# Optimization experiments

Measured on AMD Instinct MI355X. Metric: run time of the kernel, lower is better.

The kernel has to match this reference:

```python
import jax, jax.numpy as jnp
import numpy as np

B, S, D = 1, 2048, 2048
H = 16
Q_LORA = 1536
KV_LORA = 512
NOPE = 128
ROPE = 64
VD = 128
QHD = NOPE + ROPE  # 192
THETA = 50000.0
EPS = 1e-6


def rmsnorm(x, w, eps=EPS):
    xf = x.astype(jnp.float32)
    var = jnp.mean(xf * xf, axis=-1, keepdims=True)
    return (w * (xf * jax.lax.rsqrt(var + eps)).astype(x.dtype))


def rotate_half(x):
    x1, x2 = jnp.split(x, 2, axis=-1)
    return jnp.concatenate([-x2, x1], axis=-1)


def deinterleave(x):
    # view(..., d//2, 2).transpose(-1,-2).reshape(..., d): [x0,x2,...,x1,x3,...]
    b, h, s, d = x.shape
    return x.reshape(b, h, s, d // 2, 2).swapaxes(-1, -2).reshape(b, h, s, d)


def setup_inputs() -> dict:
    key = jax.random.key(0)
    ks = jax.random.split(key, 8)
    sc = 0.02
    return {
        "hidden_states": jax.random.normal(ks[0], (B, S, D), jnp.float32),
        "position_ids": jnp.broadcast_to(jnp.arange(S, dtype=jnp.int32), (B, S)),
        "q_a_w": jax.random.normal(ks[1], (Q_LORA, D), jnp.float32) * sc,
        "q_a_ln_w": jnp.ones((Q_LORA,), jnp.float32),
        "q_b_w": jax.random.normal(ks[2], (H * QHD, Q_LORA), jnp.float32) * sc,
        "kv_a_w": jax.random.normal(ks[3], (KV_LORA + ROPE, D), jnp.float32) * sc,
        "kv_a_ln_w": jnp.ones((KV_LORA,), jnp.float32),
        "kv_b_w": jax.random.normal(ks[4], (H * (NOPE + VD), KV_LORA), jnp.float32) * sc,
        "o_w": jax.random.normal(ks[5], (D, H * VD), jnp.float32) * sc,
    }


def reference(hidden_states, position_ids, q_a_w, q_a_ln_w, q_b_w, kv_a_w, kv_a_ln_w, kv_b_w, o_w):
    bsz, q_len, _ = hidden_states.shape
    # low-rank Q: q_b(rmsnorm(q_a(x)))
    q = rmsnorm(hidden_states @ q_a_w.T, q_a_ln_w) @ q_b_w.T
    q = q.reshape(bsz, q_len, H, QHD).transpose(0, 2, 1, 3)  # [b,h,s,192]
    q_nope, q_pe = q[..., :NOPE], q[..., NOPE:]
    # compressed KV + shared rope key
    ckv = hidden_states @ kv_a_w.T  # [b,s,512+64]
    compressed_kv, k_pe = ckv[..., :KV_LORA], ckv[..., KV_LORA:]
    k_pe = k_pe.reshape(bsz, q_len, 1, ROPE).transpose(0, 2, 1, 3)  # [b,1,s,64]
    kv = rmsnorm(compressed_kv, kv_a_ln_w) @ kv_b_w.T
    kv = kv.reshape(bsz, q_len, H, NOPE + VD).transpose(0, 2, 1, 3)
    k_nope, value_states = kv[..., :NOPE], kv[..., NOPE:]
    # rotary cache
    inv_freq = 1.0 / (THETA ** (jnp.arange(0, ROPE, 2, dtype=jnp.float32) / ROPE))
    t = jnp.arange(q_len, dtype=jnp.float32)
    freqs = jnp.outer(t, inv_freq)
    emb = jnp.concatenate([freqs, freqs], axis=-1)  # [s,64]
    cos = jnp.cos(emb)[position_ids][:, None]  # [b,1,s,64]
    sin = jnp.sin(emb)[position_ids][:, None]
    q_pe = deinterleave(q_pe)
    k_pe = deinterleave(k_pe)
    q_pe = q_pe * cos + rotate_half(q_pe) * sin
    k_pe = k_pe * cos + rotate_half(k_pe) * sin
    query_states = jnp.concatenate([q_nope, q_pe], axis=-1)  # [b,h,s,192]
    key_states = jnp.concatenate([k_nope, jnp.broadcast_to(k_pe, (bsz, H, q_len, ROPE))], axis=-1)
    scale = QHD ** (-0.5)
    scores = jnp.einsum('bhqd,bhkd->bhqk', query_states, key_states) * scale
    causal = jnp.tril(jnp.ones((q_len, q_len), bool))
    scores = jnp.where(causal, scores, jnp.finfo(scores.dtype).min)
    attn = jax.nn.softmax(scores, axis=-1)
    out = jnp.einsum('bhqk,bhkd->bhqd', attn, value_states)  # [b,h,s,128]
    out = out.transpose(0, 2, 1, 3).reshape(bsz, q_len, H * VD)
    return out @ o_w.T
```

## Files before the change

### kernel.cpp

```cpp
#include <hip/hip_runtime.h>
#include <hip/hip_bf16.h>
#include <cmath>

#define S_LEN 2048
#define D_MODEL 2048
#define N_HEADS 16
#define Q_LORA 1536
#define KV_LORA 512
#define NOPE 128
#define ROPE_D 64
#define VD 128
#define QHD 192
#define AC_W 2112

typedef __attribute__((ext_vector_type(8))) short bf16x8;
typedef __attribute__((ext_vector_type(4))) float f32x4;
typedef __attribute__((ext_vector_type(4))) unsigned short u16x4;

static __device__ __forceinline__ unsigned short f2u(float x) {
  union { float f; unsigned u; } v; v.f = x;
  unsigned r = v.u + 0x7fffu + ((v.u >> 16) & 1u);
  return (unsigned short)(r >> 16);
}
static __device__ __forceinline__ unsigned short f2u_fast(float x) {
  union { float f; unsigned u; } v; v.f = x;
  return (unsigned short)((v.u + 0x8000u) >> 16);
}
static __device__ __forceinline__ float u2f(unsigned short x) {
  union { unsigned u; float f; } v; v.u = ((unsigned)x) << 16;
  return v.f;
}

#define AS1 __attribute__((address_space(1)))
#define AS3 __attribute__((address_space(3)))
static __device__ __forceinline__ void gload_lds16(const unsigned short* g, unsigned short* l) {
  __builtin_amdgcn_global_load_lds((const AS1 unsigned int*)g, (AS3 unsigned int*)l, 16, 0, 0);
}

__global__ __launch_bounds__(256) void conv_all(const float* __restrict__ hidden,
                                                const float* __restrict__ qaw,
                                                const float* __restrict__ kvaw,
                                                const float* __restrict__ qbw,
                                                const float* __restrict__ kvbw,
                                                unsigned short* __restrict__ Hb,
                                                unsigned short* __restrict__ wbuf,
                                                unsigned short* __restrict__ qbwb,
                                                unsigned short* __restrict__ kvbwb,
                                                float qscale) {
  const int nH   = (S_LEN * D_MODEL) / 4;
  const int nQA  = (Q_LORA * D_MODEL) / 4;
  const int nKVA = ((KV_LORA + ROPE_D) * D_MODEL) / 4;
  const int nQB  = (N_HEADS * QHD * Q_LORA) / 4;
  const int nKVB = (N_HEADS * 256 * KV_LORA) / 4;
  const int e1 = nH, e2 = e1 + nQA + nKVA, e3 = e2 + nQB, e4 = e3 + nKVB;
  for (int i = blockIdx.x * 256 + threadIdx.x; i < e4; i += gridDim.x * 256) {
    float4 v;
    unsigned short* dst;
    int o;
    float sc = 1.f;
    if (i < e1) {
      o = i; v = ((const float4*)hidden)[o]; dst = Hb;
    } else if (i < e2) {
      o = i - e1;
      v = (o < nQA) ? ((const float4*)qaw)[o] : ((const float4*)kvaw)[o - nQA];
      dst = wbuf;
    } else if (i < e3) {
      o = i - e2; v = ((const float4*)qbw)[o]; dst = qbwb; sc = qscale;
    } else {
      o = i - e3; v = ((const float4*)kvbw)[o]; dst = kvbwb;
    }
    u16x4 u;
    u[0] = f2u(v.x * sc); u[1] = f2u(v.y * sc);
    u[2] = f2u(v.z * sc); u[3] = f2u(v.w * sc);
    ((u16x4*)dst)[o] = u;
  }
}

template <int MODE>
__global__ __launch_bounds__(256) void gemm_mfma(const unsigned short* __restrict__ A,
                                                 const unsigned short* __restrict__ W,
                                                 void* __restrict__ Cv,
                                                 int N, int K) {
  __shared__ unsigned short As[2][8192];
  __shared__ unsigned short Ws[2][4096];
  const int tid = threadIdx.x;
  const int wave = tid >> 6, lane = tid & 63;
  const int col16 = lane & 15, g = lane >> 4;
  const int arow = blockIdx.y * 128, wrow = blockIdx.x * 64;
  const int wm = (wave >> 1) * 64, wn = (wave & 1) * 32;

  const unsigned short* gA[4];
  const unsigned short* gW[2];
  int dA[4], dW[2];
#pragma unroll
  for (int i = 0; i < 4; ++i) {
    const int c = i * 256 + tid;
    const int r = c >> 3, sl = c & 7;
    gA[i] = A + (size_t)(arow + r) * K + (sl ^ (r & 7)) * 8;
    dA[i] = c * 8;
  }
#pragma unroll
  for (int i = 0; i < 2; ++i) {
    const int c = i * 256 + tid;
    const int r = c >> 3, sl = c & 7;
    gW[i] = W + (size_t)(wrow + r) * K + (sl ^ (r & 7)) * 8;
    dW[i] = c * 8;
  }

  f32x4 acc[4][2];
#pragma unroll
  for (int i = 0; i < 4; ++i)
#pragma unroll
    for (int j = 0; j < 2; ++j) acc[i][j] = (f32x4){0.f, 0.f, 0.f, 0.f};

#pragma unroll
  for (int i = 0; i < 4; ++i) gload_lds16(gA[i], &As[0][dA[i]]);
#pragma unroll
  for (int i = 0; i < 2; ++i) gload_lds16(gW[i], &Ws[0][dW[i]]);

  int cur = 0;
  for (int k0 = 0; k0 < K; k0 += 64) {
    __syncthreads();
    if (k0 + 64 < K) {
      const int b = cur ^ 1, kk = k0 + 64;
#pragma unroll
      for (int i = 0; i < 4; ++i) gload_lds16(gA[i] + kk, &As[b][dA[i]]);
#pragma unroll
      for (int i = 0; i < 2; ++i) gload_lds16(gW[i] + kk, &Ws[b][dW[i]]);
    }
#pragma unroll
    for (int kh = 0; kh < 2; ++kh) {
      bf16x8 af[4], bfr[2];
#pragma unroll
      for (int i = 0; i < 4; ++i) {
        const int row = wm + i * 16 + col16;
        af[i] = *(const bf16x8*)(&As[cur][row * 64 + (((kh * 4 + g) ^ (row & 7)) * 8)]);
      }
#pragma unroll
      for (int j = 0; j < 2; ++j) {
        const int row = wn + j * 16 + col16;
        bfr[j] = *(const bf16x8*)(&Ws[cur][row * 64 + (((kh * 4 + g) ^ (row & 7)) * 8)]);
      }
#pragma unroll
      for (int i = 0; i < 4; ++i)
#pragma unroll
        for (int j = 0; j < 2; ++j)
          acc[i][j] = __builtin_amdgcn_mfma_f32_16x16x32_bf16(af[i], bfr[j], acc[i][j], 0, 0, 0);
    }
    cur ^= 1;
  }

#pragma unroll
  for (int i = 0; i < 4; ++i)
#pragma unroll
    for (int j = 0; j < 2; ++j) {
      const int col = wrow + wn + j * 16 + col16;
      const int row0 = arow + wm + i * 16 + g * 4;
#pragma unroll
      for (int r = 0; r < 4; ++r) {
        if constexpr (MODE == 0)
          ((float*)Cv)[(size_t)(row0 + r) * N + col] = acc[i][j][r];
        else
          ((unsigned short*)Cv)[(size_t)(row0 + r) * N + col] = f2u(acc[i][j][r]);
      }
    }
}

__global__ __launch_bounds__(256) void gemm_qkv(const unsigned short* __restrict__ qan,
                                                const unsigned short* __restrict__ wq,
                                                unsigned short* __restrict__ qbuf,
                                                const unsigned short* __restrict__ ckvn,
                                                const unsigned short* __restrict__ wkv,
                                                unsigned short* __restrict__ Kb,
                                                unsigned short* __restrict__ Vt) {
  __shared__ unsigned short As[2][8192];
  __shared__ unsigned short Ws[2][4096];
  const int tid = threadIdx.x;
  const int wave = tid >> 6, lane = tid & 63;
  const int col16 = lane & 15, g = lane >> 4;
  const int bid = (int)blockIdx.x;
  const bool isQ = bid < 768;
  int bx, by;
  if (isQ) { bx = bid % 48; by = bid / 48; }
  else { const int r = bid - 768; bx = r & 63; by = r >> 6; }
  const int K = isQ ? Q_LORA : KV_LORA;
  const unsigned short* A = isQ ? qan : ckvn;
  const unsigned short* W = isQ ? wq : wkv;
  const int arow = by * 128, wrow = bx * 64;
  const int wm = (wave >> 1) * 64, wn = (wave & 1) * 32;

  const unsigned short* gA[4];
  const unsigned short* gW[2];
  int dA[4], dW[2];
#pragma unroll
  for (int i = 0; i < 4; ++i) {
    const int c = i * 256 + tid;
    const int r = c >> 3, sl = c & 7;
    gA[i] = A + (size_t)(arow + r) * K + (sl ^ (r & 7)) * 8;
    dA[i] = c * 8;
  }
#pragma unroll
  for (int i = 0; i < 2; ++i) {
    const int c = i * 256 + tid;
    const int r = c >> 3, sl = c & 7;
    gW[i] = W + (size_t)(wrow + r) * K + (sl ^ (r & 7)) * 8;
    dW[i] = c * 8;
  }

  f32x4 acc[4][2];
#pragma unroll
  for (int i = 0; i < 4; ++i)
#pragma unroll
    for (int j = 0; j < 2; ++j) acc[i][j] = (f32x4){0.f, 0.f, 0.f, 0.f};

#pragma unroll
  for (int i = 0; i < 4; ++i) gload_lds16(gA[i], &As[0][dA[i]]);
#pragma unroll
  for (int i = 0; i < 2; ++i) gload_lds16(gW[i], &Ws[0][dW[i]]);

  int cur = 0;
  for (int k0 = 0; k0 < K; k0 += 64) {
    __syncthreads();
    if (k0 + 64 < K) {
      const int b = cur ^ 1, kk = k0 + 64;
#pragma unroll
      for (int i = 0; i < 4; ++i) gload_lds16(gA[i] + kk, &As[b][dA[i]]);
#pragma unroll
      for (int i = 0; i < 2; ++i) gload_lds16(gW[i] + kk, &Ws[b][dW[i]]);
    }
#pragma unroll
    for (int kh = 0; kh < 2; ++kh) {
      bf16x8 af[4], bfr[2];
#pragma unroll
      for (int i = 0; i < 4; ++i) {
        const int row = wm + i * 16 + col16;
        af[i] = *(const bf16x8*)(&As[cur][row * 64 + (((kh * 4 + g) ^ (row & 7)) * 8)]);
      }
#pragma unroll
      for (int j = 0; j < 2; ++j) {
        const int row = wn + j * 16 + col16;
        bfr[j] = *(const bf16x8*)(&Ws[cur][row * 64 + (((kh * 4 + g) ^ (row & 7)) * 8)]);
      }
#pragma unroll
      for (int i = 0; i < 4; ++i)
#pragma unroll
        for (int j = 0; j < 2; ++j)
          acc[i][j] = __builtin_amdgcn_mfma_f32_16x16x32_bf16(af[i], bfr[j], acc[i][j], 0, 0, 0);
    }
    cur ^= 1;
  }

#pragma unroll
  for (int i = 0; i < 4; ++i)
#pragma unroll
    for (int j = 0; j < 2; ++j) {
      const int col = wrow + wn + j * 16 + col16;
      const int row0 = arow + wm + i * 16 + g * 4;
      if (isQ) {
#pragma unroll
        for (int r = 0; r < 4; ++r)
          qbuf[(size_t)(row0 + r) * (N_HEADS * QHD) + col] = f2u(acc[i][j][r]);
      } else {
        const int hh = col >> 8, d = col & 255;
        if (d < NOPE) {
#pragma unroll
          for (int r = 0; r < 4; ++r)
            Kb[((size_t)hh * S_LEN + row0 + r) * QHD + d] = f2u(acc[i][j][r]);
        } else {
          const int dv = d - NOPE;
          const int p0 = ((row0 & 15) >> 2) * 8 + ((row0 >> 4) & 1) * 4;
          u16x4 w4;
#pragma unroll
          for (int r = 0; r < 4; ++r) w4[r] = f2u(acc[i][j][r]);
          *(uint2*)(Vt + ((size_t)hh * VD + dv) * S_LEN + (row0 & ~31) + p0) =
              __builtin_bit_cast(uint2, w4);
        }
      }
    }
}

__global__ __launch_bounds__(256) void rmsnorm2_kernel(const unsigned short* __restrict__ ac,
                                                       const float* __restrict__ wq,
                                                       const float* __restrict__ wkv,
                                                       unsigned short* __restrict__ qan,
                                                       unsigned short* __restrict__ ckvn) {
  const int row = blockIdx.x;
  const bool kv = blockIdx.y != 0;
  const unsigned short* x = ac + (size_t)row * AC_W + (kv ? Q_LORA : 0);
  const float* w = kv ? wkv : wq;
  unsigned short* dst = kv ? (ckvn + (size_t)row * KV_LORA) : (qan + (size_t)row * Q_LORA);
  const int dim = kv ? KV_LORA : Q_LORA;
  float ss = 0.f;
  for (int i0 = threadIdx.x * 8; i0 < dim; i0 += 2048) {
    const bf16x8 v = *(const bf16x8*)(x + i0);
#pragma unroll
    for (int e = 0; e < 8; ++e) {
      const float f = u2f((unsigned short)v[e]);
      ss += f * f;
    }
  }
#pragma unroll
  for (int off = 32; off; off >>= 1) ss += __shfl_xor(ss, off);
  __shared__ float red[4];
  const int wv = threadIdx.x >> 6, ln = threadIdx.x & 63;
  if (ln == 0) red[wv] = ss;
  __syncthreads();
  const float tot = red[0] + red[1] + red[2] + red[3];
  const float scale = rsqrtf(tot / (float)dim + 1e-6f);
  for (int i0 = threadIdx.x * 8; i0 < dim; i0 += 2048) {
    const bf16x8 v = *(const bf16x8*)(x + i0);
    u16x4 o0, o1;
#pragma unroll
    for (int e = 0; e < 4; ++e) {
      o0[e] = f2u(w[i0 + e] * (u2f((unsigned short)v[e]) * scale));
      o1[e] = f2u(w[i0 + 4 + e] * (u2f((unsigned short)v[4 + e]) * scale));
    }
    *(uint2*)(dst + i0) = __builtin_bit_cast(uint2, o0);
    *(uint2*)(dst + i0 + 4) = __builtin_bit_cast(uint2, o1);
  }
}

__global__ __launch_bounds__(256) void rope_kernel(unsigned short* __restrict__ q,
                                                   const unsigned short* __restrict__ ac,
                                                   unsigned short* __restrict__ Kb,
                                                   const int* __restrict__ pos_ids) {
  const int s = blockIdx.x * 8 + (threadIdx.x >> 5);
  const int j = threadIdx.x & 31;
  const float t = (float)pos_ids[s];
  const float invf = powf(50000.0f, -(float)(2 * j) / 64.0f);
  const float ang = t * invf;
  const float c = cosf(ang), sn = sinf(ang);
#pragma unroll
  for (int h = 0; h < N_HEADS; ++h) {
    unsigned short* base = q + (size_t)s * (N_HEADS * QHD) + h * QHD + NOPE;
    const float x0 = u2f(base[2 * j]), x1 = u2f(base[2 * j + 1]);
    base[j] = f2u(x0 * c - x1 * sn);
    base[32 + j] = f2u(x1 * c + x0 * sn);
  }
  const unsigned short* kb = ac + (size_t)s * AC_W + 2048;
  const float kb0 = u2f(kb[2 * j]), kb1 = u2f(kb[2 * j + 1]);
  const unsigned short r0 = f2u(kb0 * c - kb1 * sn);
  const unsigned short r1 = f2u(kb1 * c + kb0 * sn);
#pragma unroll
  for (int h = 0; h < N_HEADS; ++h) {
    unsigned short* kd = Kb + ((size_t)h * S_LEN + s) * QHD + NOPE;
    kd[j] = r0;
    kd[32 + j] = r1;
  }
}

__global__ __launch_bounds__(256, 4) void flash_attn(const unsigned short* __restrict__ Q,
                                                     const unsigned short* __restrict__ Kb,
                                                     const unsigned short* __restrict__ Vt,
                                                     unsigned short* __restrict__ Pb,
                                                     float2* __restrict__ mlb) {
  __shared__ unsigned short Ks[2][32 * QHD];
  __shared__ unsigned short Vs[2][VD * 32];
  const int tid = threadIdx.x;
  const int wave = tid >> 6, lane = tid & 63;
  const int g = lane >> 4, col = lane & 15;
  const int lin = (int)blockIdx.x;
  const int h = ((lin & 7) << 1) | ((lin >> 3) & 1);
  const int s = (lin >> 4) & 1;
  const int z = lin >> 5;
  int t;
  if (z < 8) t = 31 - z;
  else if (z < 16) t = z - 8;
  else if (z < 24) t = 39 - z;
  else t = z - 16;
  const int qw = t * 64 + wave * 16;
  const int qr = qw + col;

  bf16x8 qf[6];
  {
    const unsigned short* qrow = Q + (size_t)qr * (N_HEADS * QHD) + h * QHD + g * 8;
#pragma unroll
    for (int i = 0; i < 6; ++i) qf[i] = *(const bf16x8*)(qrow + i * 32);
  }

  const unsigned short* KbH = Kb + (size_t)h * S_LEN * QHD;
  const unsigned short* VtH = Vt + (size_t)h * VD * S_LEN;

  int eK[3], eV[2];
#pragma unroll
  for (int i = 0; i < 3; ++i) {
    const int c = i * 256 + tid;
    const int r = c / 24, sl = c - r * 24;
    eK[i] = r * QHD + (((sl & 24) | ((sl & 7) ^ (r & 7)))) * 8;
  }
#pragma unroll
  for (int i = 0; i < 2; ++i) {
    const int L = i * 256 + tid;
    const int r = L >> 3, p = L & 7;
    const int px = p ^ (r & 7);
    const int d = 2 * r + (px >> 2), sl = px & 3;
    eV[i] = d * S_LEN + sl * 8;
  }

  f32x4 o[8];
#pragma unroll
  for (int i = 0; i < 8; ++i) o[i] = (f32x4){0.f, 0.f, 0.f, 0.f};
  float m = -1e30f, l = 0.f;

  const int nT = t + 1;

  {
    const unsigned short* kp = KbH + (size_t)s * 32 * QHD;
    const unsigned short* vp = VtH + s * 32;
#pragma unroll
    for (int i = 0; i < 3; ++i) gload_lds16(kp + eK[i], &Ks[0][(i * 256 + tid) * 8]);
#pragma unroll
    for (int i = 0; i < 2; ++i) gload_lds16(vp + eV[i], &Vs[0][(i * 256 + tid) * 8]);
  }

  int xK[6];
#pragma unroll
  for (int i = 0; i < 6; ++i) xK[i] = ((4 * i + g) ^ (col & 7)) * 8;
  const int rbK = col * QHD;
  const int vlane = (col >> 1) * 64 + ((((col & 1) << 2) + g) ^ (col >> 1)) * 8;

  for (int it = 0; it < nT; ++it) {
    __syncthreads();
    if (it + 1 < nT) {
      const int jn = 2 * (it + 1) + s;
      const unsigned short* kp = KbH + (size_t)jn * 32 * QHD;
      const unsigned short* vp = VtH + jn * 32;
      const int b = (it + 1) & 1;
#pragma unroll
      for (int i = 0; i < 3; ++i) gload_lds16(kp + eK[i], &Ks[b][(i * 256 + tid) * 8]);
#pragma unroll
      for (int i = 0; i < 2; ++i) gload_lds16(vp + eV[i], &Vs[b][(i * 256 + tid) * 8]);
    }
    const int k0 = 32 * (2 * it + s);
    if (k0 <= qw + 15) {
      const unsigned short* Ksc = Ks[it & 1];
      const unsigned short* Vsc = Vs[it & 1];

      f32x4 c0 = (f32x4){0.f, 0.f, 0.f, 0.f}, c1 = (f32x4){0.f, 0.f, 0.f, 0.f};
      __builtin_amdgcn_s_setprio(1);
#pragma unroll
      for (int dt = 0; dt < 6; ++dt) {
        const bf16x8 a0 = *(const bf16x8*)(Ksc + rbK + xK[dt]);
        const bf16x8 a1 = *(const bf16x8*)(Ksc + rbK + 16 * QHD + xK[dt]);
        c0 = __builtin_amdgcn_mfma_f32_16x16x32_bf16(a0, qf[dt], c0, 0, 0, 0);
        c1 = __builtin_amdgcn_mfma_f32_16x16x32_bf16(a1, qf[dt], c1, 0, 0, 0);
      }
      __builtin_amdgcn_s_setprio(0);

      if (k0 + 31 > qw) {
#pragma unroll
        for (int r = 0; r < 4; ++r) {
          const int kk = k0 + 4 * g + r;
          if (kk > qr) c0[r] = -1e30f;
          if (kk + 16 > qr) c1[r] = -1e30f;
        }
      }
      float bm = fmaxf(fmaxf(fmaxf(c0[0], c0[1]), fmaxf(c0[2], c0[3])),
                       fmaxf(fmaxf(c1[0], c1[1]), fmaxf(c1[2], c1[3])));
      bm = fmaxf(bm, __shfl_xor(bm, 16));
      bm = fmaxf(bm, __shfl_xor(bm, 32));
      const bool skip = __all(bm <= m + 8.f);
      const float mn = skip ? m : fmaxf(m, bm);
      float ps = 0.f;
      bf16x8 pb;
#pragma unroll
      for (int r = 0; r < 4; ++r) {
        const float p0 = exp2f(c0[r] - mn);
        const float p1 = exp2f(c1[r] - mn);
        ps += p0 + p1;
        pb[r] = (short)f2u_fast(p0);
        pb[4 + r] = (short)f2u_fast(p1);
      }
      ps += __shfl_xor(ps, 16);
      ps += __shfl_xor(ps, 32);
      if (skip) {
        l += ps;
      } else {
        const float corr = exp2f(m - mn);
        l = l * corr + ps;
        m = mn;
#pragma unroll
        for (int i = 0; i < 8; ++i) {
          o[i][0] *= corr; o[i][1] *= corr; o[i][2] *= corr; o[i][3] *= corr;
        }
      }
      __builtin_amdgcn_s_setprio(1);
#pragma unroll
      for (int db = 0; db < 8; ++db) {
        const bf16x8 va = *(const bf16x8*)(Vsc + db * 512 + vlane);
        o[db] = __builtin_amdgcn_mfma_f32_16x16x32_bf16(va, pb, o[db], 0, 0, 0);
      }
      __builtin_amdgcn_s_setprio(0);
    }
  }

  unsigned short* pr = Pb + (((size_t)qr * 2 + s) * N_HEADS + h) * VD;
#pragma unroll
  for (int db = 0; db < 8; ++db) {
    u16x4 w4;
#pragma unroll
    for (int r = 0; r < 4; ++r) w4[r] = f2u(o[db][r]);
    *(uint2*)(pr + db * 16 + 4 * g) = __builtin_bit_cast(uint2, w4);
  }
  if (g == 0) mlb[((size_t)qr * 2 + s) * N_HEADS + h] = make_float2(m, l);
}

__global__ __launch_bounds__(256) void combine2(const unsigned short* __restrict__ Pb,
                                                const float2* __restrict__ mlb,
                                                unsigned short* __restrict__ outb,
                                                const float* __restrict__ ow,
                                                unsigned short* __restrict__ owb) {
  const int nC = S_LEN * N_HEADS * VD / 8;
  const int nT = nC + (D_MODEL * N_HEADS * VD) / 4;
  for (int idx = blockIdx.x * 256 + threadIdx.x; idx < nT; idx += gridDim.x * 256) {
    if (idx < nC) {
      const int d8 = idx & 15, hq = idx >> 4;
      const int h = hq & 15, q = hq >> 4;
      const float2 a = mlb[((size_t)q * 2 + 0) * N_HEADS + h];
      const float2 b = mlb[((size_t)q * 2 + 1) * N_HEADS + h];
      const float M = fmaxf(a.x, b.x);
      float wA = exp2f(a.x - M), wB = exp2f(b.x - M);
      const float inv = 1.f / (wA * a.y + wB * b.y);
      wA *= inv; wB *= inv;
      const bf16x8 v0 = *(const bf16x8*)(Pb + (((size_t)q * 2 + 0) * N_HEADS + h) * VD + d8 * 8);
      const bf16x8 v1 = *(const bf16x8*)(Pb + (((size_t)q * 2 + 1) * N_HEADS + h) * VD + d8 * 8);
      u16x4 o0, o1;
#pragma unroll
      for (int e = 0; e < 4; ++e) {
        o0[e] = f2u(u2f((unsigned short)v0[e]) * wA + u2f((unsigned short)v1[e]) * wB);
        o1[e] = f2u(u2f((unsigned short)v0[4 + e]) * wA + u2f((unsigned short)v1[4 + e]) * wB);
      }
      unsigned short* dst = outb + ((size_t)q * N_HEADS + h) * VD + d8 * 8;
      *(uint2*)(dst) = __builtin_bit_cast(uint2, o0);
      *(uint2*)(dst + 4) = __builtin_bit_cast(uint2, o1);
    } else {
      const int i = idx - nC;
      const float4 v = ((const float4*)ow)[i];
      u16x4 u;
      u[0] = f2u(v.x); u[1] = f2u(v.y); u[2] = f2u(v.z); u[3] = f2u(v.w);
      ((u16x4*)owb)[i] = u;
    }
  }
}

extern "C" void kernel_launch(void* const* d_in, const int* in_sizes, int n_in,
                              void* d_out, int out_size, void* d_ws, size_t ws_size,
                              hipStream_t stream) {
  const float* hidden    = (const float*)d_in[0];
  const int*   pos       = (const int*)d_in[1];
  const float* q_a_w     = (const float*)d_in[2];
  const float* q_a_ln_w  = (const float*)d_in[3];
  const float* q_b_w     = (const float*)d_in[4];
  const float* kv_a_w    = (const float*)d_in[5];
  const float* kv_a_ln_w = (const float*)d_in[6];
  const float* kv_b_w    = (const float*)d_in[7];
  const float* o_w       = (const float*)d_in[8];
  float* out = (float*)d_out;
  (void)in_sizes; (void)n_in; (void)out_size; (void)ws_size;

  char* base = (char*)d_ws;
  unsigned short* qbuf  = (unsigned short*)(base);
  unsigned short* Pbuf  = (unsigned short*)(base + 12582912);
  unsigned short* qbwb  = (unsigned short*)(base + 12582912);
  unsigned short* acb   = (unsigned short*)(base + 29360128);
  unsigned short* qan   = (unsigned short*)(base + 46661632);
  float2*         mlb   = (float2*)(base + 46661632);
  unsigned short* ckvn  = (unsigned short*)(base + 52953088);
  unsigned short* Hb    = (unsigned short*)(base + 55050240);
  unsigned short* Vt    = (unsigned short*)(base + 55050240);
  unsigned short* wbuf  = (unsigned short*)(base + 63438848);
  unsigned short* attnb = (unsigned short*)(base + 72876032);
  unsigned short* kvbwb = (unsigned short*)(base + 72876032);
  unsigned short* Kb    = (unsigned short*)(base + 81264640);

  const dim3 b256(256);
  const float qscale = 0.07216878364870323f * 1.4426950408889634f;

  conv_all<<<2048, b256, 0, stream>>>(hidden, q_a_w, kv_a_w, q_b_w, kv_b_w,
                                      Hb, wbuf, qbwb, kvbwb, qscale);

  gemm_mfma<1><<<dim3(AC_W / 64, S_LEN / 128), b256, 0, stream>>>(Hb, wbuf, acb, AC_W, D_MODEL);

  rmsnorm2_kernel<<<dim3(S_LEN, 2), b256, 0, stream>>>(acb, q_a_ln_w, kv_a_ln_w, qan, ckvn);

  gemm_qkv<<<dim3(1792), b256, 0, stream>>>(qan, qbwb, qbuf, ckvn, kvbwb, Kb, Vt);

  rope_kernel<<<S_LEN / 8, b256, 0, stream>>>(qbuf, acb, Kb, pos);

  flash_attn<<<dim3(1024), b256, 0, stream>>>(qbuf, Kb, Vt, Pbuf, mlb);

  combine2<<<2048, b256, 0, stream>>>(Pbuf, mlb, attnb, o_w, wbuf);

  gemm_mfma<0><<<dim3(D_MODEL / 64, S_LEN / 128), b256, 0, stream>>>(attnb, wbuf, out, D_MODEL, N_HEADS * VD);
}
```

Baseline: 181.0 us.

## Move k_pe column tile of first GEMM into the q/kv-b GEMM launch

```diff
diff --git a/kernel.cpp b/kernel.cpp
--- a/kernel.cpp
+++ b/kernel.cpp
@@ -166,7 +166,10 @@
     }
 }
 
-__global__ __launch_bounds__(256) void gemm_qkv(const unsigned short* __restrict__ qan,
+__global__ __launch_bounds__(256) void gemm_qkv(const unsigned short* __restrict__ Hb,
+                                                const unsigned short* __restrict__ waw,
+                                                unsigned short* __restrict__ acb,
+                                                const unsigned short* __restrict__ qan,
                                                 const unsigned short* __restrict__ wq,
                                                 unsigned short* __restrict__ qbuf,
                                                 const unsigned short* __restrict__ ckvn,
@@ -179,13 +182,14 @@
   const int wave = tid >> 6, lane = tid & 63;
   const int col16 = lane & 15, g = lane >> 4;
   const int bid = (int)blockIdx.x;
-  const bool isQ = bid < 768;
-  int bx, by;
-  if (isQ) { bx = bid % 48; by = bid / 48; }
-  else { const int r = bid - 768; bx = r & 63; by = r >> 6; }
-  const int K = isQ ? Q_LORA : KV_LORA;
-  const unsigned short* A = isQ ? qan : ckvn;
-  const unsigned short* W = isQ ? wq : wkv;
+  int kind, bx, by;
+  if (bid < 16) { kind = 0; bx = 0; by = bid; }
+  else if (bid < 784) { kind = 1; const int r = bid - 16; bx = r % 48; by = r / 48; }
+  else { kind = 2; const int r = bid - 784; bx = r & 63; by = r >> 6; }
+  const int K = (kind == 0) ? D_MODEL : (kind == 1) ? Q_LORA : KV_LORA;
+  const unsigned short* A = (kind == 0) ? Hb : (kind == 1) ? qan : ckvn;
+  const unsigned short* W = (kind == 0) ? (waw + (size_t)2048 * D_MODEL)
+                                        : (kind == 1) ? wq : wkv;
   const int arow = by * 128, wrow = bx * 64;
   const int wm = (wave >> 1) * 64, wn = (wave & 1) * 32;
 
@@ -256,7 +260,11 @@
     for (int j = 0; j < 2; ++j) {
       const int col = wrow + wn + j * 16 + col16;
       const int row0 = arow + wm + i * 16 + g * 4;
-      if (isQ) {
+      if (kind == 0) {
+#pragma unroll
+        for (int r = 0; r < 4; ++r)
+          acb[(size_t)(row0 + r) * AC_W + 2048 + col] = f2u(acc[i][j][r]);
+      } else if (kind == 1) {
 #pragma unroll
         for (int r = 0; r < 4; ++r)
           qbuf[(size_t)(row0 + r) * (N_HEADS * QHD) + col] = f2u(acc[i][j][r]);
@@ -579,11 +587,11 @@
   conv_all<<<2048, b256, 0, stream>>>(hidden, q_a_w, kv_a_w, q_b_w, kv_b_w,
                                       Hb, wbuf, qbwb, kvbwb, qscale);
 
-  gemm_mfma<1><<<dim3(AC_W / 64, S_LEN / 128), b256, 0, stream>>>(Hb, wbuf, acb, AC_W, D_MODEL);
+  gemm_mfma<1><<<dim3(32, S_LEN / 128), b256, 0, stream>>>(Hb, wbuf, acb, AC_W, D_MODEL);
 
   rmsnorm2_kernel<<<dim3(S_LEN, 2), b256, 0, stream>>>(acb, q_a_ln_w, kv_a_ln_w, qan, ckvn);
 
-  gemm_qkv<<<dim3(1792), b256, 0, stream>>>(qan, qbwb, qbuf, ckvn, kvbwb, Kb, Vt);
+  gemm_qkv<<<dim3(1808), b256, 0, stream>>>(Hb, wbuf, acb, qan, qbwb, qbuf, ckvn, kvbwb, Kb, Vt);
 
   rope_kernel<<<S_LEN / 8, b256, 0, stream>>>(qbuf, acb, Kb, pos);
 
```

After: 184.7 us. 2.0% more time.
